# Kernel tuning notes

Hardware: AMD Instinct MI355X
Metric: run time of the kernel (lower is better)

Reference implementation:

```python
import jax, jax.numpy as jnp
import numpy as np
import math

N_HEADS = 16
DIM_MODEL = 1024
DIM_KQ = 64
DIM_V = 64
B, T = 2, 2048


def setup_inputs() -> dict:
    key = jax.random.key(0)
    ks = jax.random.split(key, 9)
    s = 1.0 / math.sqrt(DIM_MODEL)
    return {
        "x": jax.random.normal(ks[0], (B, T, DIM_MODEL), dtype=jnp.float32),
        "Wq": jax.random.normal(ks[1], (DIM_MODEL, N_HEADS * DIM_KQ), dtype=jnp.float32) * s,
        "bq": jnp.zeros((N_HEADS * DIM_KQ,), dtype=jnp.float32),
        "Wk": jax.random.normal(ks[2], (DIM_MODEL, N_HEADS * DIM_KQ), dtype=jnp.float32) * s,
        "bk": jnp.zeros((N_HEADS * DIM_KQ,), dtype=jnp.float32),
        "Wv": jax.random.normal(ks[3], (DIM_MODEL, N_HEADS * DIM_V), dtype=jnp.float32) * s,
        "bv": jnp.zeros((N_HEADS * DIM_V,), dtype=jnp.float32),
        "Wo": jax.random.normal(ks[4], (N_HEADS * DIM_V, DIM_MODEL), dtype=jnp.float32) * s,
        "bo": jnp.zeros((DIM_MODEL,), dtype=jnp.float32),
    }


def reference(x, Wq, bq, Wk, bk, Wv, bv, Wo, bo):
    b, t, _ = x.shape
    # projections, split into heads: [B, T, h, d]
    q = (x @ Wq + bq).reshape(b, t, N_HEADS, DIM_KQ)
    k = (x @ Wk + bk).reshape(b, t, N_HEADS, DIM_KQ)
    v = (x @ Wv + bv).reshape(b, t, N_HEADS, DIM_V)
    # NOTE: faithful to source einsum 'B Tq h d, B Tk h d -> B h Tk Tq'
    # scores[b, h, tk, tq] = q[b, tq] . k[b, tk]
    scores = jnp.einsum('bqhd,bkhd->bhkq', q, k)
    # softmax over the LAST axis (= query axis tq), as in the source
    attn = jax.nn.softmax(scores / math.sqrt(DIM_KQ), axis=-1)
    # source einsum 'B h Tk Tq, B Tq h dv -> B Tq h dv':
    # sums over Tk only -> out[b, tq, h, dv] = v[b, tq, h, dv] * sum_tk attn[b, h, tk, tq]
    colsum = attn.sum(axis=2)                      # [B, h, Tq]
    mixed = v * colsum.transpose(0, 2, 1)[..., None]  # [B, Tq, h, dv]
    out = mixed.reshape(b, t, N_HEADS * DIM_V) @ Wo + bo
    return out
```

## Files before the change

### kernel.cpp

```cpp
#include <hip/hip_runtime.h>
#include <hip/hip_bf16.h>
#include <stdint.h>

typedef __attribute__((ext_vector_type(4))) float f32x4;
typedef __attribute__((ext_vector_type(8))) __bf16 bf16x8;

#define AS1 __attribute__((address_space(1)))
#define AS3 __attribute__((address_space(3)))

#if __has_builtin(__builtin_amdgcn_exp2f)
#define EXP2(x) __builtin_amdgcn_exp2f(x)
#else
#define EXP2(x) exp2f(x)
#endif

__device__ __forceinline__ ushort f2bf(float f) {
  uint32_t u = __builtin_bit_cast(uint32_t, f);
  u += 0x7fffu + ((u >> 16) & 1u);
  return (ushort)(u >> 16);
}
__device__ __forceinline__ float bf2f(ushort h) {
  uint32_t u = ((uint32_t)h) << 16;
  return __builtin_bit_cast(float, u);
}

#define SCK 0.18033688011112042f

#define GLD(src, dst) \
  __builtin_amdgcn_global_load_lds((const AS1 uint32_t*)(src), (AS3 uint32_t*)(dst), 16, 0, 0)

#define BARRIER()                          \
  do {                                     \
    __builtin_amdgcn_sched_barrier(0);     \
    __builtin_amdgcn_s_barrier();          \
    __builtin_amdgcn_sched_barrier(0);     \
  } while (0)


__global__ void k_prep(const float* __restrict__ x, const float* __restrict__ Wq,
                       const float* __restrict__ Wk, const float* __restrict__ Wv,
                       const float* __restrict__ Wo, ushort* __restrict__ xb,
                       ushort* __restrict__ Wt, ushort* __restrict__ Wot) {
  __shared__ float tile[32][33];
  int z = blockIdx.z;
  int tx = threadIdx.x, ty = threadIdx.y;
  if (z == 4) {
    int base = (blockIdx.y * 32 + blockIdx.x) * 256 + ty * 32 + tx;
#pragma unroll
    for (int i = 0; i < 4; i++) {
      int idx = base + i * 262144;
      float4 v = ((const float4*)x)[idx];
      ushort4 o;
      o.x = f2bf(v.x); o.y = f2bf(v.y); o.z = f2bf(v.z); o.w = f2bf(v.w);
      ((ushort4*)xb)[idx] = o;
    }
    return;
  }
  const float* src = (z == 0) ? Wq : (z == 1) ? Wk : (z == 2) ? Wv : Wo;
  ushort* dst = (z < 3) ? (Wt + (size_t)z * 1048576) : Wot;
  float scale = (z == 1) ? SCK : 1.0f;
  int k0 = blockIdx.y * 32, n0 = blockIdx.x * 32;
#pragma unroll
  for (int i = 0; i < 4; i++)
    tile[ty + i * 8][tx] = src[(size_t)(k0 + ty + i * 8) * 1024 + n0 + tx];
  __syncthreads();
#pragma unroll
  for (int i = 0; i < 4; i++)
    dst[(size_t)(n0 + ty + i * 8) * 1024 + k0 + tx] = f2bf(tile[tx][ty + i * 8] * scale);
}

__global__ __launch_bounds__(256, 3) void k_gemm_qkv(const ushort* __restrict__ A,
                                                     const ushort* __restrict__ Bt,
                                                     ushort* __restrict__ C,
                                                     const float* __restrict__ b0,
                                                     const float* __restrict__ b1,
                                                     const float* __restrict__ b2) {
  __shared__ ushort As[128 * 64];
  __shared__ ushort Bs[128 * 64];
  const int K = 1024, ldc = 3072;
  const int tid = threadIdx.x;
  const int lane = tid & 63;
  const int wid = tid >> 6;
  const int wr = wid >> 1, wc = wid & 1;
  const int l15 = lane & 15, l4 = lane >> 4;

  const int chunk = (int)gridDim.x >> 3;
  const int L = blockIdx.x;
  const int f = (L & 7) * chunk + (L >> 3);
  const int row0 = (f & 31) * 128;
  const int col0 = (f >> 5) * 128;
  const int T = K >> 6;

  const int rt = tid >> 3;
  const int cswz = ((tid & 7) ^ (rt & 7)) * 8;
  const ushort* Ap = A + (size_t)(row0 + rt) * K + cswz;
  const ushort* Bp = Bt + (size_t)(col0 + rt) * K + cswz;

  int aoff[4][2], boff[4][2];
#pragma unroll
  for (int m = 0; m < 4; m++) {
    int r = wr * 64 + m * 16 + l15;
#pragma unroll
    for (int ks = 0; ks < 2; ks++)
      aoff[m][ks] = r * 128 + (((ks * 4 + l4) ^ (r & 7)) << 4);
  }
#pragma unroll
  for (int n = 0; n < 4; n++) {
    int r = wc * 64 + n * 16 + l15;
#pragma unroll
    for (int ks = 0; ks < 2; ks++)
      boff[n][ks] = r * 128 + (((ks * 4 + l4) ^ (r & 7)) << 4);
  }

  f32x4 acc[4][4] = {};

  for (int t = 0; t < T; ++t) {
#pragma unroll
    for (int i = 0; i < 4; i++)
      GLD(Ap + (size_t)(32 * i) * K + t * 64, (char*)As + (i * 256 + tid) * 16);
#pragma unroll
    for (int i = 0; i < 4; i++)
      GLD(Bp + (size_t)(32 * i) * K + t * 64, (char*)Bs + (i * 256 + tid) * 16);
    asm volatile("s_waitcnt vmcnt(0)" ::: "memory");
    BARRIER();

    bf16x8 af[4][2], bf_[4][2];
#pragma unroll
    for (int m = 0; m < 4; m++)
#pragma unroll
      for (int ks = 0; ks < 2; ks++)
        af[m][ks] = *(const bf16x8*)((const char*)As + aoff[m][ks]);
#pragma unroll
    for (int n = 0; n < 4; n++)
#pragma unroll
      for (int ks = 0; ks < 2; ks++)
        bf_[n][ks] = *(const bf16x8*)((const char*)Bs + boff[n][ks]);

    __builtin_amdgcn_s_setprio(1);
#pragma unroll
    for (int m = 0; m < 4; m++)
#pragma unroll
      for (int n = 0; n < 4; n++)
#pragma unroll
        for (int ks = 0; ks < 2; ks++)
          acc[m][n] = __builtin_amdgcn_mfma_f32_16x16x32_bf16(af[m][ks], bf_[n][ks],
                                                              acc[m][n], 0, 0, 0);
    __builtin_amdgcn_s_setprio(0);
    BARRIER();
  }

#pragma unroll
  for (int m = 0; m < 4; m++)
#pragma unroll
    for (int n = 0; n < 4; n++) {
      int colg = col0 + wc * 64 + n * 16 + l15;
      float bias = (colg < 1024) ? b0[colg]
                                 : ((colg < 2048) ? b1[colg - 1024] * SCK : b2[colg - 2048]);
#pragma unroll
      for (int j = 0; j < 4; j++) {
        int rowg = row0 + wr * 64 + m * 16 + l4 * 4 + j;
        C[(size_t)rowg * ldc + colg] = f2bf(acc[m][n][j] + bias);
      }
    }
}

__global__ __launch_bounds__(256, 2) void k_gemm_out(const ushort* __restrict__ QKV,
                                                     const float* __restrict__ csPart,
                                                     const ushort* __restrict__ Wot,
                                                     float* __restrict__ out,
                                                     const float* __restrict__ bo) {
  __shared__ ushort As[2][128 * 64];
  __shared__ ushort Bs[2][64 * 64];
  const int tid = threadIdx.x;
  const int lane = tid & 63;
  const int wid = tid >> 6;
  const int wr = wid >> 1, wc = wid & 1;
  const int l15 = lane & 15, l4 = lane >> 4;

  const int L = blockIdx.x;
  const int f = (L & 7) * 64 + (L >> 3);
  const int row0 = (f & 31) * 128;
  const int col0 = (f >> 5) * 64;

  const int rt = tid >> 3, sl = tid & 7;
  int grow[4], gbh[4];
#pragma unroll
  for (int i = 0; i < 4; i++) {
    grow[i] = row0 + 32 * i + rt;
    gbh[i] = ((grow[i] >> 11) << 4) * 2048 + (grow[i] & 2047);
  }

  uint4 av[4];
  float csv[4];

#define ISSUE(t)                                                                   \
  do {                                                                             \
    _Pragma("unroll") for (int i = 0; i < 2; i++) {                                \
      int c = i * 256 + tid;                                                       \
      int rb = c >> 3;                                                             \
      GLD(Wot + (size_t)(col0 + rb) * 1024 + (t) * 64 + (((c & 7) ^ (rb & 7)) * 8),\
          (char*)Bs[(t) & 1] + c * 16);                                            \
    }                                                                              \
    _Pragma("unroll") for (int i = 0; i < 4; i++)                                  \
        av[i] = *(const uint4*)(QKV + (size_t)grow[i] * 3072 + 2048 + (t) * 64 +   \
                                sl * 8);                                           \
    _Pragma("unroll") for (int i = 0; i < 4; i++) {                                \
      int g = gbh[i] + (t) * 2048;                                                 \
      csv[i] = csPart[g] + csPart[65536 + g];                                      \
    }                                                                              \
  } while (0)

#define WRITE_A(t)                                                                 \
  do {                                                                             \
    _Pragma("unroll") for (int i = 0; i < 4; i++) {                                \
      int r = 32 * i + rt;                                                         \
      const ushort* pv = (const ushort*)&av[i];                                    \
      ushort o[8];                                                                 \
      _Pragma("unroll") for (int k = 0; k < 8; k++)                                \
          o[k] = f2bf(bf2f(pv[k]) * csv[i]);                                       \
      *(uint4*)((char*)As[(t) & 1] + r * 128 + ((sl ^ (r & 7)) << 4)) =            \
          *(const uint4*)o;                                                        \
    }                                                                              \
  } while (0)

  int aoff[4][2], boff[2][2];
#pragma unroll
  for (int m = 0; m < 4; m++) {
    int r = wr * 64 + m * 16 + l15;
#pragma unroll
    for (int ks = 0; ks < 2; ks++)
      aoff[m][ks] = r * 128 + (((ks * 4 + l4) ^ (r & 7)) << 4);
  }
#pragma unroll
  for (int n = 0; n < 2; n++) {
    int r = wc * 32 + n * 16 + l15;
#pragma unroll
    for (int ks = 0; ks < 2; ks++)
      boff[n][ks] = r * 128 + (((ks * 4 + l4) ^ (r & 7)) << 4);
  }

  f32x4 acc[4][2] = {};

  ISSUE(0);
  asm volatile("s_waitcnt vmcnt(0)" ::: "memory");
  WRITE_A(0);
  asm volatile("s_waitcnt lgkmcnt(0)" ::: "memory");
  BARRIER();

  for (int t = 0; t < 16; ++t) {
    if (t < 15) ISSUE(t + 1);
    __builtin_amdgcn_sched_barrier(0);
    const char* Ab = (const char*)As[t & 1];
    const char* Bb = (const char*)Bs[t & 1];
    bf16x8 af[4][2], bf_[2][2];
#pragma unroll
    for (int m = 0; m < 4; m++)
#pragma unroll
      for (int ks = 0; ks < 2; ks++)
        af[m][ks] = *(const bf16x8*)(Ab + aoff[m][ks]);
#pragma unroll
    for (int n = 0; n < 2; n++)
#pragma unroll
      for (int ks = 0; ks < 2; ks++)
        bf_[n][ks] = *(const bf16x8*)(Bb + boff[n][ks]);
    __builtin_amdgcn_s_setprio(1);
#pragma unroll
    for (int m = 0; m < 4; m++)
#pragma unroll
      for (int n = 0; n < 2; n++)
#pragma unroll
        for (int ks = 0; ks < 2; ks++)
          acc[m][n] = __builtin_amdgcn_mfma_f32_16x16x32_bf16(af[m][ks], bf_[n][ks],
                                                              acc[m][n], 0, 0, 0);
    __builtin_amdgcn_s_setprio(0);
    if (t < 15) {
      asm volatile("s_waitcnt vmcnt(0)" ::: "memory");
      WRITE_A(t + 1);
      asm volatile("s_waitcnt lgkmcnt(0)" ::: "memory");
    }
    BARRIER();
  }

#undef ISSUE
#undef WRITE_A

#pragma unroll
  for (int m = 0; m < 4; m++)
#pragma unroll
    for (int n = 0; n < 2; n++) {
      int colg = col0 + wc * 32 + n * 16 + l15;
      float bias = bo[colg];
#pragma unroll
      for (int j = 0; j < 4; j++) {
        int rowg = row0 + wr * 64 + m * 16 + l4 * 4 + j;
        out[(size_t)rowg * 1024 + colg] = acc[m][n][j] + bias;
      }
    }
}

__global__ __launch_bounds__(256, 2) void k_attn_z(const ushort* __restrict__ QKV,
                                                   float* __restrict__ Zpart) {
  const int bid = blockIdx.x;
  const int xcd = bid & 7, kk = bid >> 3;
  const int g = xcd * 8 + (kk >> 3);
  const int tkb = kk & 7;
  const int bh = g & 31, s = g >> 5;
  const int b = bh >> 4, h = bh & 15;
  const int tid = threadIdx.x, lane = tid & 63, w = tid >> 6;
  const int l15 = lane & 15, l4 = lane >> 4;
  const size_t rs = 3072;

  __shared__ ushort Ks[256 * 64];
  __shared__ ushort Qs[3][128 * 64];

  const ushort* Kbase = QKV + (size_t)(b * 2048 + tkb * 256) * rs + 1024 + h * 64;
  const ushort* Qbase = QKV + (size_t)(b * 2048 + s * 1024) * rs + h * 64;

  const int csl = ((tid & 7) ^ ((tid >> 3) & 7)) * 8;

#pragma unroll
  for (int i = 0; i < 8; i++) {
    int c = i * 256 + tid;
    GLD(Kbase + (size_t)(c >> 3) * rs + csl, (char*)Ks + c * 16);
  }
  const ushort* gq[4];
#pragma unroll
  for (int i = 0; i < 4; i++) {
    int c = i * 256 + tid;
    gq[i] = Qbase + (size_t)(c >> 3) * rs + csl;
    GLD(gq[i], (char*)Qs[0] + c * 16);
  }
#pragma unroll
  for (int i = 0; i < 4; i++) {
    int c = i * 256 + tid;
    GLD(gq[i] + 128 * rs, (char*)Qs[1] + c * 16);
  }
  asm volatile("s_waitcnt vmcnt(4)" ::: "memory");
  BARRIER();

  bf16x8 kf[4][2];
#pragma unroll
  for (int m = 0; m < 4; m++)
#pragma unroll
    for (int d = 0; d < 2; d++) {
      int r = w * 64 + m * 16 + l15;
      kf[m][d] = *(const bf16x8*)((const char*)Ks + r * 128 + (((d * 4 + l4) ^ (r & 7)) << 4));
    }

  float z[4][4] = {};
  const f32x4 zero4 = {0.f, 0.f, 0.f, 0.f};

  for (int t = 0; t < 8; ++t) {
    if (t + 2 < 8) {
      char* qd = (char*)Qs[(t + 2) % 3];
#pragma unroll
      for (int i = 0; i < 4; i++) {
        int c = i * 256 + tid;
        GLD(gq[i] + (size_t)(t + 2) * 128 * rs, qd + c * 16);
      }
    }
    const char* qb = (const char*)Qs[t % 3];
    f32x4 acc[4][8];
    __builtin_amdgcn_s_setprio(1);
#pragma unroll
    for (int d = 0; d < 2; d++)
#pragma unroll
      for (int n = 0; n < 8; n++) {
        int r = n * 16 + l15;
        bf16x8 qf = *(const bf16x8*)(qb + r * 128 + (((d * 4 + l4) ^ (r & 7)) << 4));
#pragma unroll
        for (int m = 0; m < 4; m++)
          acc[m][n] = __builtin_amdgcn_mfma_f32_16x16x32_bf16(
              kf[m][d], qf, d == 0 ? zero4 : acc[m][n], 0, 0, 0);
      }
    __builtin_amdgcn_s_setprio(0);
#pragma unroll
    for (int m = 0; m < 4; m++)
#pragma unroll
      for (int n = 0; n < 8; n++)
#pragma unroll
        for (int j = 0; j < 4; j++) z[m][j] += EXP2(acc[m][n][j]);
    if (t < 6) {
      asm volatile("s_waitcnt vmcnt(4)" ::: "memory");
      BARRIER();
    } else if (t == 6) {
      asm volatile("s_waitcnt vmcnt(0)" ::: "memory");
      BARRIER();
    }
  }

#pragma unroll
  for (int m = 0; m < 4; m++)
#pragma unroll
    for (int j = 0; j < 4; j++) {
      float v = z[m][j];
      v += __shfl_xor(v, 1, 64);
      v += __shfl_xor(v, 2, 64);
      v += __shfl_xor(v, 4, 64);
      v += __shfl_xor(v, 8, 64);
      if (l15 == 0)
        Zpart[(size_t)s * 65536 + bh * 2048 + tkb * 256 + w * 64 + m * 16 + l4 * 4 + j] = v;
    }
}

__global__ __launch_bounds__(256, 2) void k_attn_cs(const ushort* __restrict__ QKV,
                                                    const float* __restrict__ Zpart,
                                                    float* __restrict__ csPart) {
  const int bid = blockIdx.x;
  const int xcd = bid & 7, kk = bid >> 3;
  const int g = xcd * 8 + (kk >> 3);
  const int tqb = kk & 7;
  const int bh = g & 31, s = g >> 5;
  const int b = bh >> 4, h = bh & 15;
  const int tid = threadIdx.x, lane = tid & 63, w = tid >> 6;
  const int l15 = lane & 15, l4 = lane >> 4;
  const size_t rs = 3072;

  __shared__ ushort Qs[256 * 64];
  __shared__ ushort Ks[3][128 * 64];

  const ushort* Qbase = QKV + (size_t)(b * 2048 + tqb * 256) * rs + h * 64;
  const ushort* Kbase = QKV + (size_t)(b * 2048 + s * 1024) * rs + 1024 + h * 64;
  const float* zp = Zpart + bh * 2048 + s * 1024;

  const int csl = ((tid & 7) ^ ((tid >> 3) & 7)) * 8;

#pragma unroll
  for (int i = 0; i < 8; i++) {
    int c = i * 256 + tid;
    GLD(Qbase + (size_t)(c >> 3) * rs + csl, (char*)Qs + c * 16);
  }
  const ushort* gk[4];
#pragma unroll
  for (int i = 0; i < 4; i++) {
    int c = i * 256 + tid;
    gk[i] = Kbase + (size_t)(c >> 3) * rs + csl;
    GLD(gk[i], (char*)Ks[0] + c * 16);
  }
#pragma unroll
  for (int i = 0; i < 4; i++) {
    int c = i * 256 + tid;
    GLD(gk[i] + 128 * rs, (char*)Ks[1] + c * 16);
  }
  asm volatile("s_waitcnt vmcnt(4)" ::: "memory");
  BARRIER();

  bf16x8 qf[4][2];
#pragma unroll
  for (int m = 0; m < 4; m++)
#pragma unroll
    for (int d = 0; d < 2; d++) {
      int r = w * 64 + m * 16 + l15;
      qf[m][d] = *(const bf16x8*)((const char*)Qs + r * 128 + (((d * 4 + l4) ^ (r & 7)) << 4));
    }

  float cs[4][4] = {};
  const f32x4 zero4 = {0.f, 0.f, 0.f, 0.f};

  for (int t = 0; t < 8; ++t) {
    float rz[8];
#pragma unroll
    for (int n = 0; n < 8; n++) {
      int idx = t * 128 + n * 16 + l15;
      rz[n] = 1.0f / (zp[idx] + zp[65536 + idx]);
    }
    if (t + 2 < 8) {
      char* kd = (char*)Ks[(t + 2) % 3];
#pragma unroll
      for (int i = 0; i < 4; i++) {
        int c = i * 256 + tid;
        GLD(gk[i] + (size_t)(t + 2) * 128 * rs, kd + c * 16);
      }
    }
    const char* kb = (const char*)Ks[t % 3];
    f32x4 acc[4][8];
    __builtin_amdgcn_s_setprio(1);
#pragma unroll
    for (int d = 0; d < 2; d++)
#pragma unroll
      for (int n = 0; n < 8; n++) {
        int r = n * 16 + l15;
        bf16x8 kft = *(const bf16x8*)(kb + r * 128 + (((d * 4 + l4) ^ (r & 7)) << 4));
#pragma unroll
        for (int m = 0; m < 4; m++)
          acc[m][n] = __builtin_amdgcn_mfma_f32_16x16x32_bf16(
              qf[m][d], kft, d == 0 ? zero4 : acc[m][n], 0, 0, 0);
      }
    __builtin_amdgcn_s_setprio(0);
#pragma unroll
    for (int m = 0; m < 4; m++)
#pragma unroll
      for (int n = 0; n < 8; n++)
#pragma unroll
        for (int j = 0; j < 4; j++)
          cs[m][j] = fmaf(EXP2(acc[m][n][j]), rz[n], cs[m][j]);
    if (t < 6) {
      asm volatile("s_waitcnt vmcnt(4)" ::: "memory");
      BARRIER();
    } else if (t == 6) {
      asm volatile("s_waitcnt vmcnt(0)" ::: "memory");
      BARRIER();
    }
  }

#pragma unroll
  for (int m = 0; m < 4; m++)
#pragma unroll
    for (int j = 0; j < 4; j++) {
      float v = cs[m][j];
      v += __shfl_xor(v, 1, 64);
      v += __shfl_xor(v, 2, 64);
      v += __shfl_xor(v, 4, 64);
      v += __shfl_xor(v, 8, 64);
      if (l15 == 0)
        csPart[(size_t)s * 65536 + bh * 2048 + tqb * 256 + w * 64 + m * 16 + l4 * 4 + j] = v;
    }
}


extern "C" void kernel_launch(void* const* d_in, const int* in_sizes, int n_in,
                              void* d_out, int out_size, void* d_ws, size_t ws_size,
                              hipStream_t stream) {
  const float* x = (const float*)d_in[0];
  const float* Wq = (const float*)d_in[1];
  const float* bq = (const float*)d_in[2];
  const float* Wk = (const float*)d_in[3];
  const float* bk = (const float*)d_in[4];
  const float* Wv = (const float*)d_in[5];
  const float* bv = (const float*)d_in[6];
  const float* Wo = (const float*)d_in[7];
  const float* bo = (const float*)d_in[8];

  char* ws = (char*)d_ws;
  ushort* xb     = (ushort*)(ws);
  ushort* Wt     = (ushort*)(ws + 8388608);
  ushort* Wot    = (ushort*)(ws + 14680064);
  ushort* QKV    = (ushort*)(ws + 16777216);
  float* Zpart   = (float*)(ws + 41943040);
  float* csPart  = (float*)(ws + 42467328);

  k_prep<<<dim3(32, 32, 5), dim3(32, 8), 0, stream>>>(x, Wq, Wk, Wv, Wo, xb, Wt, Wot);
  k_gemm_qkv<<<768, 256, 0, stream>>>(xb, Wt, QKV, bq, bk, bv);
  k_attn_z<<<512, 256, 0, stream>>>(QKV, Zpart);
  k_attn_cs<<<512, 256, 0, stream>>>(QKV, Zpart, csPart);
  k_gemm_out<<<512, 256, 0, stream>>>(QKV, csPart, Wot, (float*)d_out, bo);
}
```

Baseline: 121.5 us.

## Fuse softmax-normalizer and column-sum attention passes into one kernel

Replaces the two attention kernels (row-normalizer Z, then column sums) with one kernel. Each block owns a 128-row tk tile for one head and sweeps all query tiles twice: first to compute the full-row Z, then to recompute scores and accumulate normalized column sums. Per-tk-block partials go to a [bh, tq, 16] buffer that the output GEMM reduces with vector loads. This removes a kernel launch and the Z round-trip through global memory, but recomputes QK^T and adds a shared-memory reduction with a __syncthreads in every second-pass iteration.

```diff
diff --git a/kernel.cpp b/kernel.cpp
--- a/kernel.cpp
+++ b/kernel.cpp
@@ -164,6 +164,139 @@
     }
 }
 
+__global__ __launch_bounds__(256, 2) void k_attn(const ushort* __restrict__ QKV,
+                                                 float* __restrict__ partial) {
+  const int bid = blockIdx.x;
+  const int xcd = bid & 7, idx = bid >> 3;
+  const int bh = xcd * 4 + (idx >> 4);
+  const int tkb = idx & 15;
+  const int b = bh >> 4, h = bh & 15;
+  const int tid = threadIdx.x, lane = tid & 63, w = tid >> 6;
+  const int l15 = lane & 15, l4 = lane >> 4;
+  const size_t rs = 3072;
+
+  __shared__ ushort Ks[128 * 64];
+  __shared__ ushort Qs[3][128 * 64];
+  __shared__ float colred[4][128];
+
+  const ushort* Kbase = QKV + (size_t)(b * 2048 + tkb * 128) * rs + 1024 + h * 64;
+  const ushort* Qbase = QKV + (size_t)(b * 2048) * rs + h * 64;
+  const int csl = ((tid & 7) ^ ((tid >> 3) & 7)) * 8;
+
+#pragma unroll
+  for (int i = 0; i < 4; i++) {
+    int c = i * 256 + tid;
+    GLD(Kbase + (size_t)(c >> 3) * rs + csl, (char*)Ks + c * 16);
+  }
+  const ushort* gq[4];
+#pragma unroll
+  for (int i = 0; i < 4; i++) {
+    int c = i * 256 + tid;
+    gq[i] = Qbase + (size_t)(c >> 3) * rs + csl;
+    GLD(gq[i], (char*)Qs[0] + c * 16);
+  }
+#pragma unroll
+  for (int i = 0; i < 4; i++) {
+    int c = i * 256 + tid;
+    GLD(gq[i] + 128 * rs, (char*)Qs[1] + c * 16);
+  }
+  asm volatile("s_waitcnt vmcnt(4)" ::: "memory");
+  BARRIER();
+
+  bf16x8 kf[2][2];
+#pragma unroll
+  for (int m = 0; m < 2; m++)
+#pragma unroll
+    for (int d = 0; d < 2; d++) {
+      int r = w * 32 + m * 16 + l15;
+      kf[m][d] = *(const bf16x8*)((const char*)Ks + r * 128 + (((d * 4 + l4) ^ (r & 7)) << 4));
+    }
+
+  float z[2][4] = {};
+  float rrz[2][4];
+  const f32x4 zero4 = {0.f, 0.f, 0.f, 0.f};
+
+  for (int u = 0; u < 32; ++u) {
+    if (u + 2 < 32) {
+      int qt = (u + 2) & 15;
+      char* qd = (char*)Qs[(u + 2) % 3];
+#pragma unroll
+      for (int i = 0; i < 4; i++) {
+        int c = i * 256 + tid;
+        GLD(gq[i] + (size_t)qt * 128 * rs, qd + c * 16);
+      }
+    }
+    const char* qb = (const char*)Qs[u % 3];
+    f32x4 acc[2][8];
+    __builtin_amdgcn_s_setprio(1);
+#pragma unroll
+    for (int d = 0; d < 2; d++)
+#pragma unroll
+      for (int n = 0; n < 8; n++) {
+        int r = n * 16 + l15;
+        bf16x8 qf = *(const bf16x8*)(qb + r * 128 + (((d * 4 + l4) ^ (r & 7)) << 4));
+#pragma unroll
+        for (int m = 0; m < 2; m++)
+          acc[m][n] = __builtin_amdgcn_mfma_f32_16x16x32_bf16(
+              kf[m][d], qf, d == 0 ? zero4 : acc[m][n], 0, 0, 0);
+      }
+    __builtin_amdgcn_s_setprio(0);
+
+    if (u < 16) {
+#pragma unroll
+      for (int m = 0; m < 2; m++)
+#pragma unroll
+        for (int n = 0; n < 8; n++)
+#pragma unroll
+          for (int j = 0; j < 4; j++) z[m][j] += EXP2(acc[m][n][j]);
+      if (u == 15) {
+#pragma unroll
+        for (int m = 0; m < 2; m++)
+#pragma unroll
+          for (int j = 0; j < 4; j++) {
+            float v = z[m][j];
+            v += __shfl_xor(v, 1, 64);
+            v += __shfl_xor(v, 2, 64);
+            v += __shfl_xor(v, 4, 64);
+            v += __shfl_xor(v, 8, 64);
+            rrz[m][j] = 1.0f / v;
+          }
+      }
+    } else {
+      float val[8];
+#pragma unroll
+      for (int n = 0; n < 8; n++) {
+        float s = 0.f;
+#pragma unroll
+        for (int m = 0; m < 2; m++)
+#pragma unroll
+          for (int j = 0; j < 4; j++)
+            s = fmaf(EXP2(acc[m][n][j]), rrz[m][j], s);
+        s += __shfl_xor(s, 16, 64);
+        s += __shfl_xor(s, 32, 64);
+        val[n] = s;
+      }
+      if (lane < 16) {
+#pragma unroll
+        for (int n = 0; n < 8; n++) colred[w][n * 16 + lane] = val[n];
+      }
+      __syncthreads();
+      if (tid < 128) {
+        float s = colred[0][tid] + colred[1][tid] + colred[2][tid] + colred[3][tid];
+        partial[(((size_t)bh * 2048 + (u - 16) * 128 + tid) << 4) + tkb] = s;
+      }
+    }
+
+    if (u < 30) {
+      asm volatile("s_waitcnt vmcnt(4)" ::: "memory");
+      BARRIER();
+    } else if (u == 30) {
+      asm volatile("s_waitcnt vmcnt(0)" ::: "memory");
+      BARRIER();
+    }
+  }
+}
+
 __global__ __launch_bounds__(256, 2) void k_gemm_out(const ushort* __restrict__ QKV,
                                                      const float* __restrict__ csPart,
                                                      const ushort* __restrict__ Wot,
@@ -205,8 +338,11 @@
         av[i] = *(const uint4*)(QKV + (size_t)grow[i] * 3072 + 2048 + (t) * 64 +   \
                                 sl * 8);                                           \
     _Pragma("unroll") for (int i = 0; i < 4; i++) {                                \
-      int g = gbh[i] + (t) * 2048;                                                 \
-      csv[i] = csPart[g] + csPart[65536 + g];                                      \
+      size_t g16 = ((size_t)(gbh[i] + (t) * 2048)) << 4;                           \
+      const float4* pp = (const float4*)(csPart + g16);                            \
+      float4 p0 = pp[0], p1 = pp[1], p2 = pp[2], p3 = pp[3];                       \
+      csv[i] = (((p0.x + p0.y) + (p0.z + p0.w)) + ((p1.x + p1.y) + (p1.z + p1.w))) \
+             + (((p2.x + p2.y) + (p2.z + p2.w)) + ((p3.x + p3.y) + (p3.z + p3.w)));\
     }                                                                              \
   } while (0)
 
@@ -298,225 +434,6 @@
     }
 }
 
-__global__ __launch_bounds__(256, 2) void k_attn_z(const ushort* __restrict__ QKV,
-                                                   float* __restrict__ Zpart) {
-  const int bid = blockIdx.x;
-  const int xcd = bid & 7, kk = bid >> 3;
-  const int g = xcd * 8 + (kk >> 3);
-  const int tkb = kk & 7;
-  const int bh = g & 31, s = g >> 5;
-  const int b = bh >> 4, h = bh & 15;
-  const int tid = threadIdx.x, lane = tid & 63, w = tid >> 6;
-  const int l15 = lane & 15, l4 = lane >> 4;
-  const size_t rs = 3072;
-
-  __shared__ ushort Ks[256 * 64];
-  __shared__ ushort Qs[3][128 * 64];
-
-  const ushort* Kbase = QKV + (size_t)(b * 2048 + tkb * 256) * rs + 1024 + h * 64;
-  const ushort* Qbase = QKV + (size_t)(b * 2048 + s * 1024) * rs + h * 64;
-
-  const int csl = ((tid & 7) ^ ((tid >> 3) & 7)) * 8;
-
-#pragma unroll
-  for (int i = 0; i < 8; i++) {
-    int c = i * 256 + tid;
-    GLD(Kbase + (size_t)(c >> 3) * rs + csl, (char*)Ks + c * 16);
-  }
-  const ushort* gq[4];
-#pragma unroll
-  for (int i = 0; i < 4; i++) {
-    int c = i * 256 + tid;
-    gq[i] = Qbase + (size_t)(c >> 3) * rs + csl;
-    GLD(gq[i], (char*)Qs[0] + c * 16);
-  }
-#pragma unroll
-  for (int i = 0; i < 4; i++) {
-    int c = i * 256 + tid;
-    GLD(gq[i] + 128 * rs, (char*)Qs[1] + c * 16);
-  }
-  asm volatile("s_waitcnt vmcnt(4)" ::: "memory");
-  BARRIER();
-
-  bf16x8 kf[4][2];
-#pragma unroll
-  for (int m = 0; m < 4; m++)
-#pragma unroll
-    for (int d = 0; d < 2; d++) {
-      int r = w * 64 + m * 16 + l15;
-      kf[m][d] = *(const bf16x8*)((const char*)Ks + r * 128 + (((d * 4 + l4) ^ (r & 7)) << 4));
-    }
-
-  float z[4][4] = {};
-  const f32x4 zero4 = {0.f, 0.f, 0.f, 0.f};
-
-  for (int t = 0; t < 8; ++t) {
-    if (t + 2 < 8) {
-      char* qd = (char*)Qs[(t + 2) % 3];
-#pragma unroll
-      for (int i = 0; i < 4; i++) {
-        int c = i * 256 + tid;
-        GLD(gq[i] + (size_t)(t + 2) * 128 * rs, qd + c * 16);
-      }
-    }
-    const char* qb = (const char*)Qs[t % 3];
-    f32x4 acc[4][8];
-    __builtin_amdgcn_s_setprio(1);
-#pragma unroll
-    for (int d = 0; d < 2; d++)
-#pragma unroll
-      for (int n = 0; n < 8; n++) {
-        int r = n * 16 + l15;
-        bf16x8 qf = *(const bf16x8*)(qb + r * 128 + (((d * 4 + l4) ^ (r & 7)) << 4));
-#pragma unroll
-        for (int m = 0; m < 4; m++)
-          acc[m][n] = __builtin_amdgcn_mfma_f32_16x16x32_bf16(
-              kf[m][d], qf, d == 0 ? zero4 : acc[m][n], 0, 0, 0);
-      }
-    __builtin_amdgcn_s_setprio(0);
-#pragma unroll
-    for (int m = 0; m < 4; m++)
-#pragma unroll
-      for (int n = 0; n < 8; n++)
-#pragma unroll
-        for (int j = 0; j < 4; j++) z[m][j] += EXP2(acc[m][n][j]);
-    if (t < 6) {
-      asm volatile("s_waitcnt vmcnt(4)" ::: "memory");
-      BARRIER();
-    } else if (t == 6) {
-      asm volatile("s_waitcnt vmcnt(0)" ::: "memory");
-      BARRIER();
-    }
-  }
-
-#pragma unroll
-  for (int m = 0; m < 4; m++)
-#pragma unroll
-    for (int j = 0; j < 4; j++) {
-      float v = z[m][j];
-      v += __shfl_xor(v, 1, 64);
-      v += __shfl_xor(v, 2, 64);
-      v += __shfl_xor(v, 4, 64);
-      v += __shfl_xor(v, 8, 64);
-      if (l15 == 0)
-        Zpart[(size_t)s * 65536 + bh * 2048 + tkb * 256 + w * 64 + m * 16 + l4 * 4 + j] = v;
-    }
-}
-
-__global__ __launch_bounds__(256, 2) void k_attn_cs(const ushort* __restrict__ QKV,
-                                                    const float* __restrict__ Zpart,
-                                                    float* __restrict__ csPart) {
-  const int bid = blockIdx.x;
-  const int xcd = bid & 7, kk = bid >> 3;
-  const int g = xcd * 8 + (kk >> 3);
-  const int tqb = kk & 7;
-  const int bh = g & 31, s = g >> 5;
-  const int b = bh >> 4, h = bh & 15;
-  const int tid = threadIdx.x, lane = tid & 63, w = tid >> 6;
-  const int l15 = lane & 15, l4 = lane >> 4;
-  const size_t rs = 3072;
-
-  __shared__ ushort Qs[256 * 64];
-  __shared__ ushort Ks[3][128 * 64];
-
-  const ushort* Qbase = QKV + (size_t)(b * 2048 + tqb * 256) * rs + h * 64;
-  const ushort* Kbase = QKV + (size_t)(b * 2048 + s * 1024) * rs + 1024 + h * 64;
-  const float* zp = Zpart + bh * 2048 + s * 1024;
-
-  const int csl = ((tid & 7) ^ ((tid >> 3) & 7)) * 8;
-
-#pragma unroll
-  for (int i = 0; i < 8; i++) {
-    int c = i * 256 + tid;
-    GLD(Qbase + (size_t)(c >> 3) * rs + csl, (char*)Qs + c * 16);
-  }
-  const ushort* gk[4];
-#pragma unroll
-  for (int i = 0; i < 4; i++) {
-    int c = i * 256 + tid;
-    gk[i] = Kbase + (size_t)(c >> 3) * rs + csl;
-    GLD(gk[i], (char*)Ks[0] + c * 16);
-  }
-#pragma unroll
-  for (int i = 0; i < 4; i++) {
-    int c = i * 256 + tid;
-    GLD(gk[i] + 128 * rs, (char*)Ks[1] + c * 16);
-  }
-  asm volatile("s_waitcnt vmcnt(4)" ::: "memory");
-  BARRIER();
-
-  bf16x8 qf[4][2];
-#pragma unroll
-  for (int m = 0; m < 4; m++)
-#pragma unroll
-    for (int d = 0; d < 2; d++) {
-      int r = w * 64 + m * 16 + l15;
-      qf[m][d] = *(const bf16x8*)((const char*)Qs + r * 128 + (((d * 4 + l4) ^ (r & 7)) << 4));
-    }
-
-  float cs[4][4] = {};
-  const f32x4 zero4 = {0.f, 0.f, 0.f, 0.f};
-
-  for (int t = 0; t < 8; ++t) {
-    float rz[8];
-#pragma unroll
-    for (int n = 0; n < 8; n++) {
-      int idx = t * 128 + n * 16 + l15;
-      rz[n] = 1.0f / (zp[idx] + zp[65536 + idx]);
-    }
-    if (t + 2 < 8) {
-      char* kd = (char*)Ks[(t + 2) % 3];
-#pragma unroll
-      for (int i = 0; i < 4; i++) {
-        int c = i * 256 + tid;
-        GLD(gk[i] + (size_t)(t + 2) * 128 * rs, kd + c * 16);
-      }
-    }
-    const char* kb = (const char*)Ks[t % 3];
-    f32x4 acc[4][8];
-    __builtin_amdgcn_s_setprio(1);
-#pragma unroll
-    for (int d = 0; d < 2; d++)
-#pragma unroll
-      for (int n = 0; n < 8; n++) {
-        int r = n * 16 + l15;
-        bf16x8 kft = *(const bf16x8*)(kb + r * 128 + (((d * 4 + l4) ^ (r & 7)) << 4));
-#pragma unroll
-        for (int m = 0; m < 4; m++)
-          acc[m][n] = __builtin_amdgcn_mfma_f32_16x16x32_bf16(
-              qf[m][d], kft, d == 0 ? zero4 : acc[m][n], 0, 0, 0);
-      }
-    __builtin_amdgcn_s_setprio(0);
-#pragma unroll
-    for (int m = 0; m < 4; m++)
-#pragma unroll
-      for (int n = 0; n < 8; n++)
-#pragma unroll
-        for (int j = 0; j < 4; j++)
-          cs[m][j] = fmaf(EXP2(acc[m][n][j]), rz[n], cs[m][j]);
-    if (t < 6) {
-      asm volatile("s_waitcnt vmcnt(4)" ::: "memory");
-      BARRIER();
-    } else if (t == 6) {
-      asm volatile("s_waitcnt vmcnt(0)" ::: "memory");
-      BARRIER();
-    }
-  }
-
-#pragma unroll
-  for (int m = 0; m < 4; m++)
-#pragma unroll
-    for (int j = 0; j < 4; j++) {
-      float v = cs[m][j];
-      v += __shfl_xor(v, 1, 64);
-      v += __shfl_xor(v, 2, 64);
-      v += __shfl_xor(v, 4, 64);
-      v += __shfl_xor(v, 8, 64);
-      if (l15 == 0)
-        csPart[(size_t)s * 65536 + bh * 2048 + tqb * 256 + w * 64 + m * 16 + l4 * 4 + j] = v;
-    }
-}
-
 
 extern "C" void kernel_launch(void* const* d_in, const int* in_sizes, int n_in,
                               void* d_out, int out_size, void* d_ws, size_t ws_size,
@@ -536,12 +453,10 @@
   ushort* Wt     = (ushort*)(ws + 8388608);
   ushort* Wot    = (ushort*)(ws + 14680064);
   ushort* QKV    = (ushort*)(ws + 16777216);
-  float* Zpart   = (float*)(ws + 41943040);
-  float* csPart  = (float*)(ws + 42467328);
+  float* partial = (float*)(ws + 41943040);
 
   k_prep<<<dim3(32, 32, 5), dim3(32, 8), 0, stream>>>(x, Wq, Wk, Wv, Wo, xb, Wt, Wot);
   k_gemm_qkv<<<768, 256, 0, stream>>>(xb, Wt, QKV, bq, bk, bv);
-  k_attn_z<<<512, 256, 0, stream>>>(QKV, Zpart);
-  k_attn_cs<<<512, 256, 0, stream>>>(QKV, Zpart, csPart);
-  k_gemm_out<<<512, 256, 0, stream>>>(QKV, csPart, Wot, (float*)d_out, bo);
-}
+  k_attn<<<512, 256, 0, stream>>>(QKV, partial);
+  k_gemm_out<<<512, 256, 0, stream>>>(QKV, partial, Wot, (float*)d_out, bo);
+}
```

Result: slower. 131.5 us (+8.2%).
